# Kernel optimization log

Hardware: AMD Instinct MI355X
Metric: run time of the kernel (lower is better)

Reference implementation:

```python
import jax, jax.numpy as jnp
import numpy as np
import math

B, S, D, H = 2, 2048, 1024, 16
DH = D // H  # dim_per_head = 64


def setup_inputs() -> dict:
    key = jax.random.key(0)
    ks = jax.random.split(key, 12)
    s = 1.0 / math.sqrt(D)
    return {
        "key": jax.random.normal(ks[0], (B, S, D), jnp.float32),
        "value": jax.random.normal(ks[1], (B, S, D), jnp.float32),
        "query": jax.random.normal(ks[2], (B, S, D), jnp.float32),
        "mask": jax.random.randint(ks[3], (B, S, S), 0, 2).astype(bool),
        "Wq": jax.random.normal(ks[4], (D, D), jnp.float32) * s,
        "bq": jnp.zeros((D,), jnp.float32),
        "Wk": jax.random.normal(ks[5], (D, D), jnp.float32) * s,
        "bk": jnp.zeros((D,), jnp.float32),
        "Wv": jax.random.normal(ks[6], (D, D), jnp.float32) * s,
        "bv": jnp.zeros((D,), jnp.float32),
        "Wo": jax.random.normal(ks[7], (D, D), jnp.float32) * s,
        "bo": jnp.zeros((D,), jnp.float32),
    }


def _shape(x):
    # [B, S, D] -> [B, H, S, DH]
    return x.reshape(B, -1, H, DH).transpose(0, 2, 1, 3)


def reference(key, value, query, mask, Wq, bq, Wk, bk, Wv, bv, Wo, bo):
    q = _shape(query @ Wq.T + bq)  # [B,H,Sq,DH]
    k = _shape(key @ Wk.T + bk)    # [B,H,Sk,DH]
    v = _shape(value @ Wv.T + bv)  # [B,H,Sk,DH]
    q = q / jnp.sqrt(jnp.asarray(DH, q.dtype))
    scores = jnp.einsum("bhqd,bhkd->bhqk", q, k)
    scores = jnp.where(mask[:, None, :, :], jnp.asarray(-1e18, scores.dtype), scores)
    attn = jax.nn.softmax(scores, axis=-1)
    # dropout is identity in eval/deterministic reference
    ctx = jnp.einsum("bhqk,bhkd->bhqd", attn, v)
    ctx = ctx.transpose(0, 2, 1, 3).reshape(B, -1, D)  # unshape
    return ctx @ Wo.T + bo
```

## Files before the change

kernel.cpp:

```cpp
#include <hip/hip_runtime.h>
#include <math.h>


constexpr int Bc  = 2;
constexpr int Sc  = 2048;
constexpr int Dc  = 1024;
constexpr int Hc  = 16;
constexpr int DHc = 64;
constexpr int BSc = Bc * Sc;

constexpr float LOG2E = 1.4426950408889634f;

typedef __bf16 bf16x8 __attribute__((ext_vector_type(8)));
typedef __bf16 bf16x4 __attribute__((ext_vector_type(4)));
typedef __bf16 bf16x2 __attribute__((ext_vector_type(2)));
typedef float  f32x4  __attribute__((ext_vector_type(4)));
typedef float  f32x16 __attribute__((ext_vector_type(16)));
typedef unsigned uint32x2 __attribute__((ext_vector_type(2)));
typedef unsigned uint32x4 __attribute__((ext_vector_type(4)));

#define GLDS16(gp, lp) __builtin_amdgcn_global_load_lds( \
    (const __attribute__((address_space(1))) void*)(gp), \
    (__attribute__((address_space(3))) void*)(lp), 16, 0, 0)

__global__ __launch_bounds__(256)
void wsplit(const float* __restrict__ W0, const float* __restrict__ W1,
            const float* __restrict__ W2, const float* __restrict__ W3,
            __bf16* __restrict__ out, __bf16* __restrict__ out2)
{
    const float* src[4] = {W0, W1, W2, W3};
    const int z = blockIdx.y;
    const size_t idx = ((size_t)blockIdx.x * 256 + threadIdx.x) * 4;
    const float4 v = *(const float4*)&src[z][idx];
    if (z == 3) {
        bf16x8 o;
        o[0] = (__bf16)v.x; o[1] = (__bf16)v.x;
        o[2] = (__bf16)v.y; o[3] = (__bf16)v.y;
        o[4] = (__bf16)v.z; o[5] = (__bf16)v.z;
        o[6] = (__bf16)v.w; o[7] = (__bf16)v.w;
        *(bf16x8*)&out2[idx * 2] = o;
    } else {
        bf16x4 o;
        o[0] = (__bf16)v.x; o[1] = (__bf16)v.y; o[2] = (__bf16)v.z; o[3] = (__bf16)v.w;
        *(bf16x4*)&out[(size_t)z * Dc * Dc + idx] = o;
    }
}

__global__ __launch_bounds__(256)
void acast(const float* __restrict__ A0, const float* __restrict__ A1,
           const float* __restrict__ A2, __bf16* __restrict__ out)
{
    const float* src[3] = {A0, A1, A2};
    const int z = blockIdx.y;
    const size_t idx = ((size_t)blockIdx.x * 256 + threadIdx.x) * 8;
    const float4 a = *(const float4*)&src[z][idx];
    const float4 b = *(const float4*)&src[z][idx + 4];
    bf16x8 o;
    o[0] = (__bf16)a.x; o[1] = (__bf16)a.y; o[2] = (__bf16)a.z; o[3] = (__bf16)a.w;
    o[4] = (__bf16)b.x; o[5] = (__bf16)b.y; o[6] = (__bf16)b.z; o[7] = (__bf16)b.w;
    *(bf16x8*)&out[(size_t)z * BSc * Dc + idx] = o;
}

template<int KD>
__device__ __forceinline__ void sweep128bb(const __bf16* __restrict__ A,
                                           const __bf16* __restrict__ Wh,
                                           char* AsB, char* WsB,
                                           int gm0, int gn0, f32x4 acc[4][4])
{
    const int tid  = threadIdx.x;
    const int w    = tid >> 6;
    const int lane = tid & 63;
    const int cc   = lane & 15;
    const int g    = lane >> 4;
    const int wm   = (w & 1) * 64;
    const int wn   = (w >> 1) * 64;

    int wrow[4], wchk[4];
#pragma unroll
    for (int r = 0; r < 4; ++r) {
        const int L = r * 256 + tid;
        wrow[r] = L >> 3;
        wchk[r] = (L & 7) ^ (wrow[r] & 7);
    }

#pragma unroll
    for (int r = 0; r < 4; ++r) {
        GLDS16(Wh + (size_t)(gn0 + wrow[r]) * KD + wchk[r] * 8,
               WsB + (r * 256 + tid) * 16);
        GLDS16(A + (size_t)(gm0 + wrow[r]) * KD + wchk[r] * 8,
               AsB + (r * 256 + tid) * 16);
    }

    for (int it = 0; it < KD / 64; ++it) {
        const char* As = AsB + (it & 1) * 16384;
        const char* Ws = WsB + (it & 1) * 16384;
        __syncthreads();

        if (it + 1 < KD / 64) {
            const int kn = (it + 1) * 64;
            char* Wn = WsB + ((it + 1) & 1) * 16384;
            char* An = AsB + ((it + 1) & 1) * 16384;
#pragma unroll
            for (int r = 0; r < 4; ++r) {
                GLDS16(Wh + (size_t)(gn0 + wrow[r]) * KD + kn + wchk[r] * 8,
                       Wn + (r * 256 + tid) * 16);
                GLDS16(A + (size_t)(gm0 + wrow[r]) * KD + kn + wchk[r] * 8,
                       An + (r * 256 + tid) * 16);
            }
        }

        __builtin_amdgcn_s_setprio(1);
#pragma unroll
        for (int kk = 0; kk < 2; ++kk) {
            const int cb4 = (kk * 4 + g) << 4;
            bf16x8 af[4], bfr[4];
#pragma unroll
            for (int mt = 0; mt < 4; ++mt) {
                const int row = wm + mt * 16 + cc;
                af[mt] = *(const bf16x8*)(As + row * 128 + (cb4 ^ ((row & 7) << 4)));
            }
#pragma unroll
            for (int nt = 0; nt < 4; ++nt) {
                const int row = wn + nt * 16 + cc;
                bfr[nt] = *(const bf16x8*)(Ws + row * 128 + (cb4 ^ ((row & 7) << 4)));
            }
#pragma unroll
            for (int mt = 0; mt < 4; ++mt)
#pragma unroll
                for (int nt = 0; nt < 4; ++nt)
                    acc[mt][nt] = __builtin_amdgcn_mfma_f32_16x16x32_bf16(
                        af[mt], bfr[nt], acc[mt][nt], 0, 0, 0);
        }
        __builtin_amdgcn_s_setprio(0);
    }
}

__global__ __launch_bounds__(256)
void qkv_mfma(const __bf16* __restrict__ Abf, const __bf16* __restrict__ Whi,
              const float* __restrict__ bq, const float* __restrict__ bk,
              const float* __restrict__ bv,
              __bf16* __restrict__ Qo, __bf16* __restrict__ Ko, __bf16* __restrict__ Vt)
{
    __shared__ __align__(16) char smem[65536];

    const int z = blockIdx.z;
    const float* bias = (z == 0) ? bq : (z == 1) ? bk : bv;
    const float scale = (z == 0) ? 0.125f * LOG2E : 1.0f;
    const __bf16* A   = Abf + (size_t)z * BSc * Dc;
    const __bf16* Wh  = Whi + (size_t)z * Dc * Dc;

    const int gm0 = blockIdx.x * 128;
    const int gn0 = blockIdx.y * 128;

    f32x4 acc[4][4];
#pragma unroll
    for (int mt = 0; mt < 4; ++mt)
#pragma unroll
        for (int nt = 0; nt < 4; ++nt) acc[mt][nt] = {0.f, 0.f, 0.f, 0.f};

    sweep128bb<Dc>(A, Wh, smem, smem + 32768, gm0, gn0, acc);

    const int tid = threadIdx.x;
    const int w = tid >> 6, lane = tid & 63;
    const int cc = lane & 15, g = lane >> 4;
    const int wm = (w & 1) * 64, wn = (w >> 1) * 64;

    float bias4[4];
#pragma unroll
    for (int nt = 0; nt < 4; ++nt) bias4[nt] = bias[gn0 + wn + nt * 16 + cc];

    if (z == 2) {
#pragma unroll
        for (int mt = 0; mt < 4; ++mt)
#pragma unroll
            for (int nt = 0; nt < 4; ++nt) {
                const int col = gn0 + wn + nt * 16 + cc;
                const int h = col >> 6, dh = col & 63;
                const int row0 = gm0 + wm + mt * 16 + g * 4;
                const int b = row0 >> 11, s0 = row0 & 2047;
                bf16x4 vv;
#pragma unroll
                for (int reg = 0; reg < 4; ++reg)
                    vv[reg] = (__bf16)(acc[mt][nt][reg] + bias4[nt]);
                *(bf16x4*)&Vt[(((size_t)(b * Hc + h)) * DHc + dh) * Sc + s0] = vv;
            }
    } else {
        __bf16* O = (z == 0) ? Qo : Ko;
#pragma unroll
        for (int mt = 0; mt < 4; ++mt)
#pragma unroll
            for (int nt = 0; nt < 4; ++nt) {
                const int col = gn0 + wn + nt * 16 + cc;
                const int h = col >> 6, dh = col & 63;
#pragma unroll
                for (int reg = 0; reg < 4; ++reg) {
                    const int row = gm0 + wm + mt * 16 + g * 4 + reg;
                    const int b = row >> 11, s = row & 2047;
                    O[(((size_t)(b * Hc + h)) * Sc + s) * DHc + dh] =
                        (__bf16)((acc[mt][nt][reg] + bias4[nt]) * scale);
                }
            }
    }
}

__global__ __launch_bounds__(256)
void out_mfma(const __bf16* __restrict__ ctx2, const __bf16* __restrict__ Wo2,
              const float* __restrict__ bo, float* __restrict__ out)
{
    __shared__ __align__(16) char smem[65536];

    const int gm0 = blockIdx.x * 128;
    const int gn0 = blockIdx.y * 128;

    f32x4 acc[4][4];
#pragma unroll
    for (int mt = 0; mt < 4; ++mt)
#pragma unroll
        for (int nt = 0; nt < 4; ++nt) acc[mt][nt] = {0.f, 0.f, 0.f, 0.f};

    sweep128bb<2 * Dc>(ctx2, Wo2, smem, smem + 32768, gm0, gn0, acc);

    const int tid = threadIdx.x;
    const int w = tid >> 6, lane = tid & 63;
    const int cc = lane & 15, g = lane >> 4;
    const int wm = (w & 1) * 64, wn = (w >> 1) * 64;

    float bias4[4];
#pragma unroll
    for (int nt = 0; nt < 4; ++nt) bias4[nt] = bo[gn0 + wn + nt * 16 + cc];

#pragma unroll
    for (int mt = 0; mt < 4; ++mt)
#pragma unroll
        for (int nt = 0; nt < 4; ++nt) {
            const int col = gn0 + wn + nt * 16 + cc;
#pragma unroll
            for (int reg = 0; reg < 4; ++reg) {
                const int row = gm0 + wm + mt * 16 + g * 4 + reg;
                out[(size_t)row * Dc + col] = acc[mt][nt][reg] + bias4[nt];
            }
        }
}

__global__ __launch_bounds__(256)
void mask_pack(const int* __restrict__ mask, unsigned long long* __restrict__ out)
{
    const int lane = threadIdx.x & 63;
    const size_t waveBase = ((size_t)blockIdx.x * 4 + (threadIdx.x >> 6)) * 256;
    unsigned long long b0 = __ballot(mask[waveBase + lane]        != 0);
    unsigned long long b1 = __ballot(mask[waveBase + 64 + lane]   != 0);
    unsigned long long b2 = __ballot(mask[waveBase + 128 + lane]  != 0);
    unsigned long long b3 = __ballot(mask[waveBase + 192 + lane]  != 0);
    if (lane == 0) {
        unsigned long long* dst = out + (waveBase >> 6);
        dst[0] = b0; dst[1] = b1; dst[2] = b2; dst[3] = b3;
    }
}

__global__ __launch_bounds__(256, 2)
void attn_mfma(const __bf16* __restrict__ Q, const __bf16* __restrict__ K,
               const __bf16* __restrict__ Vt,
               const unsigned long long* __restrict__ mp,
               __bf16* __restrict__ ctx2)
{
    __shared__ __align__(16) char smem[32768];

    const int tid  = threadIdx.x;
    const int w    = tid >> 6;
    const int lane = tid & 63;
    const int c    = lane & 31;
    const int u    = lane >> 5;
    const int bh   = blockIdx.y;
    const int b    = bh >> 4;
    const int h    = bh & 15;
    const int qw   = blockIdx.x * 128 + w * 32;

    const __bf16* Qb  = Q  + (size_t)bh * Sc * DHc;
    const __bf16* Kb  = K  + (size_t)bh * Sc * DHc;
    const __bf16* Vtb = Vt + (size_t)bh * DHc * Sc;

    bf16x8 qa[4];
#pragma unroll
    for (int ch = 0; ch < 4; ++ch)
        qa[ch] = *(const bf16x8*)&Qb[(size_t)(qw + c) * DHc + ch * 16 + u * 8];

    f32x16 o[2];
#pragma unroll
    for (int dt = 0; dt < 2; ++dt)
#pragma unroll
        for (int i = 0; i < 16; ++i) o[dt][i] = 0.f;
    float lp[4] = {0.f, 0.f, 0.f, 0.f};

    const int ci[2] = {tid, 256 + tid};
    int rowi[2], ski[2];
#pragma unroll
    for (int i = 0; i < 2; ++i) {
        rowi[i] = ci[i] >> 3;
        ski[i]  = (ci[i] & 7) ^ (rowi[i] & 7);
    }

#pragma unroll
    for (int i = 0; i < 2; ++i) {
        GLDS16(Kb + (size_t)rowi[i] * DHc + ski[i] * 8,
               smem + ci[i] * 16);
        GLDS16(Vtb + (size_t)rowi[i] * Sc + ski[i] * 8,
               smem + 8192 + ci[i] * 16);
    }

    for (int it = 0; it < 32; ++it) {
        const char* Ks = smem + (it & 1) * 16384;
        const char* Vs = Ks + 8192;

        __syncthreads();

        if (it + 1 < 32) {
            char* Kn = smem + ((it + 1) & 1) * 16384;
            const int kn = (it + 1) * 64;
#pragma unroll
            for (int i = 0; i < 2; ++i) {
                GLDS16(Kb + (size_t)(kn + rowi[i]) * DHc + ski[i] * 8,
                       Kn + ci[i] * 16);
                GLDS16(Vtb + (size_t)rowi[i] * Sc + kn + ski[i] * 8,
                       Kn + 8192 + ci[i] * 16);
            }
        }

        const unsigned long long mw =
            mp[((size_t)(b * Sc + qw + c) << 5) + it];

        f32x16 sc[2];
        __builtin_amdgcn_s_setprio(1);
#pragma unroll
        for (int nt = 0; nt < 2; ++nt) {
            f32x16 z;
#pragma unroll
            for (int i = 0; i < 16; ++i) z[i] = -24.f;
#pragma unroll
            for (int ch = 0; ch < 4; ++ch) {
                const int row = nt * 32 + c;
                const bf16x8 kb = *(const bf16x8*)
                    (Ks + row * 128 + ((ch * 32 + u * 16) ^ ((row & 7) << 4)));
                z = __builtin_amdgcn_mfma_f32_32x32x16_bf16(kb, qa[ch], z, 0, 0, 0);
            }
            sc[nt] = z;
        }
        __builtin_amdgcn_s_setprio(0);

        unsigned pk[2][4][2];
#pragma unroll
        for (int nt = 0; nt < 2; ++nt)
#pragma unroll
            for (int rr = 0; rr < 4; ++rr) {
                const unsigned nib =
                    (unsigned)(mw >> (nt * 32 + rr * 8 + u * 4)) & 0xFu;
                float pv[4];
#pragma unroll
                for (int r = 0; r < 4; ++r) {
                    float p = __builtin_amdgcn_exp2f(sc[nt][rr * 4 + r]);
                    p = (nib & (1u << r)) ? 0.f : p;
                    lp[rr] += p;
                    pv[r] = p;
                }
                bf16x2 t0; t0[0] = (__bf16)pv[0]; t0[1] = (__bf16)pv[1];
                bf16x2 t1; t1[0] = (__bf16)pv[2]; t1[1] = (__bf16)pv[3];
                pk[nt][rr][0] = __builtin_bit_cast(unsigned, t0);
                pk[nt][rr][1] = __builtin_bit_cast(unsigned, t1);
            }

        bf16x8 pa[4];
#pragma unroll
        for (int kc = 0; kc < 4; ++kc) {
            const int nt = kc >> 1;
            const int r0 = (kc & 1) * 2;
            uint32x2 s0 = __builtin_amdgcn_permlane32_swap(
                pk[nt][r0][0], pk[nt][r0 + 1][0], false, false);
            uint32x2 s1 = __builtin_amdgcn_permlane32_swap(
                pk[nt][r0][1], pk[nt][r0 + 1][1], false, false);
            uint32x4 wds;
            wds[0] = s0[0]; wds[1] = s1[0]; wds[2] = s0[1]; wds[3] = s1[1];
            pa[kc] = __builtin_bit_cast(bf16x8, wds);
        }

        __builtin_amdgcn_s_setprio(1);
#pragma unroll
        for (int dt = 0; dt < 2; ++dt)
#pragma unroll
            for (int kc = 0; kc < 4; ++kc) {
                const int row = dt * 32 + c;
                const bf16x8 vb = *(const bf16x8*)
                    (Vs + row * 128 + ((kc * 32 + u * 16) ^ ((row & 7) << 4)));
                o[dt] = __builtin_amdgcn_mfma_f32_32x32x16_bf16(pa[kc], vb, o[dt], 0, 0, 0);
            }
        __builtin_amdgcn_s_setprio(0);
    }

    float lsum = (lp[0] + lp[1]) + (lp[2] + lp[3]);
    lsum += __shfl_xor(lsum, 32);
    const float linv = 1.0f / lsum;

    float inv[16];
#pragma unroll
    for (int i = 0; i < 16; ++i)
        inv[i] = __shfl(linv, (i & 3) + 8 * (i >> 2) + 4 * u);

#pragma unroll
    for (int dt = 0; dt < 2; ++dt)
#pragma unroll
        for (int i = 0; i < 16; ++i) {
            const int q = qw + (i & 3) + 8 * (i >> 2) + 4 * u;
            const int col = h * 64 + dt * 32 + c;
            const float v = o[dt][i] * inv[i];
            const __bf16 hi = (__bf16)v;
            bf16x2 hv;
            hv[0] = hi;
            hv[1] = (__bf16)(v - (float)hi);
            *(bf16x2*)&ctx2[(((size_t)b * Sc + q) * Dc + col) * 2] = hv;
        }
}

extern "C" void kernel_launch(void* const* d_in, const int* in_sizes, int n_in,
                              void* d_out, int out_size, void* d_ws, size_t ws_size,
                              hipStream_t stream)
{
    const float* key   = (const float*)d_in[0];
    const float* value = (const float*)d_in[1];
    const float* query = (const float*)d_in[2];
    const int*   mask  = (const int*)  d_in[3];
    const float* Wq    = (const float*)d_in[4];
    const float* bq    = (const float*)d_in[5];
    const float* Wk    = (const float*)d_in[6];
    const float* bk    = (const float*)d_in[7];
    const float* Wv    = (const float*)d_in[8];
    const float* bv    = (const float*)d_in[9];
    const float* Wo    = (const float*)d_in[10];
    const float* bo    = (const float*)d_in[11];
    float* out = (float*)d_out;

    char* wsb = (char*)d_ws;
    __bf16* Qbf  = (__bf16*)(wsb);
    __bf16* Kbf  = (__bf16*)(wsb + ((size_t)8  << 20));
    __bf16* Vt   = (__bf16*)(wsb + ((size_t)16 << 20));
    unsigned long long* mpk = (unsigned long long*)(wsb + ((size_t)24 << 20));
    __bf16* Whi  = (__bf16*)(wsb + ((size_t)25 << 20));
    __bf16* Wo2  = (__bf16*)(wsb + ((size_t)31 << 20));
    __bf16* ctx2 = (__bf16*)(wsb + ((size_t)35 << 20));
    __bf16* Abf  = (__bf16*)(wsb + ((size_t)51 << 20));

    dim3 gws(Dc * Dc / (256 * 4), 4);
    wsplit<<<gws, 256, 0, stream>>>(Wq, Wk, Wv, Wo, Whi, Wo2);

    dim3 gac(BSc * Dc / (256 * 8), 3);
    acast<<<gac, 256, 0, stream>>>(query, key, value, Abf);

    dim3 gqkv(BSc / 128, Dc / 128, 3);
    qkv_mfma<<<gqkv, 256, 0, stream>>>(Abf, Whi, bq, bk, bv, Qbf, Kbf, Vt);

    const int mask_n = Bc * Sc * Sc;
    mask_pack<<<mask_n / 1024, 256, 0, stream>>>(mask, mpk);

    dim3 gattn(Sc / 128, Bc * Hc);
    attn_mfma<<<gattn, 256, 0, stream>>>(Qbf, Kbf, Vt, mpk, ctx2);

    dim3 gout(BSc / 128, Dc / 128);
    out_mfma<<<gout, 256, 0, stream>>>(ctx2, Wo2, bo, out);
}
```

Baseline: 268.1 us.

## Use 64-row tiles for output GEMM and split MFMA accumulator chains in attention

The output projection moves from 128x128 to 64x128 tiles through a new sweep64bb helper, which doubles the block count (256 to 512) for better CU occupancy on the K=2048 GEMM. In the attention kernel, the QK^T and PV MFMA chains are split across two independent accumulators that are summed afterwards, so dependent MFMAs can overlap. The cost is more reloading of the weight tile across blocks and extra accumulator registers, which may reduce attention occupancy.

```diff
diff --git a/kernel.cpp b/kernel.cpp
--- a/kernel.cpp
+++ b/kernel.cpp
@@ -135,6 +135,89 @@
     }
 }
 
+template<int KD>
+__device__ __forceinline__ void sweep64bb(const __bf16* __restrict__ A,
+                                          const __bf16* __restrict__ Wh,
+                                          char* AsB, char* WsB,
+                                          int gm0, int gn0, f32x4 acc[2][4])
+{
+    const int tid  = threadIdx.x;
+    const int w    = tid >> 6;
+    const int lane = tid & 63;
+    const int cc   = lane & 15;
+    const int g    = lane >> 4;
+    const int wm   = (w & 1) * 32;
+    const int wn   = (w >> 1) * 64;
+
+    int wrow[4], wchk[4];
+#pragma unroll
+    for (int r = 0; r < 4; ++r) {
+        const int L = r * 256 + tid;
+        wrow[r] = L >> 3;
+        wchk[r] = (L & 7) ^ (wrow[r] & 7);
+    }
+    int arow[2], achk[2];
+#pragma unroll
+    for (int r = 0; r < 2; ++r) {
+        const int L = r * 256 + tid;
+        arow[r] = L >> 3;
+        achk[r] = (L & 7) ^ (arow[r] & 7);
+    }
+
+#pragma unroll
+    for (int r = 0; r < 4; ++r)
+        GLDS16(Wh + (size_t)(gn0 + wrow[r]) * KD + wchk[r] * 8,
+               WsB + (r * 256 + tid) * 16);
+#pragma unroll
+    for (int r = 0; r < 2; ++r)
+        GLDS16(A + (size_t)(gm0 + arow[r]) * KD + achk[r] * 8,
+               AsB + (r * 256 + tid) * 16);
+
+    for (int it = 0; it < KD / 64; ++it) {
+        const char* As = AsB + (it & 1) * 8192;
+        const char* Ws = WsB + (it & 1) * 16384;
+        __syncthreads();
+
+        if (it + 1 < KD / 64) {
+            const int kn = (it + 1) * 64;
+            char* Wn = WsB + ((it + 1) & 1) * 16384;
+            char* An = AsB + ((it + 1) & 1) * 8192;
+#pragma unroll
+            for (int r = 0; r < 4; ++r)
+                GLDS16(Wh + (size_t)(gn0 + wrow[r]) * KD + kn + wchk[r] * 8,
+                       Wn + (r * 256 + tid) * 16);
+#pragma unroll
+            for (int r = 0; r < 2; ++r)
+                GLDS16(A + (size_t)(gm0 + arow[r]) * KD + kn + achk[r] * 8,
+                       An + (r * 256 + tid) * 16);
+        }
+
+        __builtin_amdgcn_s_setprio(1);
+#pragma unroll
+        for (int kk = 0; kk < 2; ++kk) {
+            const int cb4 = (kk * 4 + g) << 4;
+            bf16x8 af[2], bfr[4];
+#pragma unroll
+            for (int mt = 0; mt < 2; ++mt) {
+                const int row = wm + mt * 16 + cc;
+                af[mt] = *(const bf16x8*)(As + row * 128 + (cb4 ^ ((row & 7) << 4)));
+            }
+#pragma unroll
+            for (int nt = 0; nt < 4; ++nt) {
+                const int row = wn + nt * 16 + cc;
+                bfr[nt] = *(const bf16x8*)(Ws + row * 128 + (cb4 ^ ((row & 7) << 4)));
+            }
+#pragma unroll
+            for (int mt = 0; mt < 2; ++mt)
+#pragma unroll
+                for (int nt = 0; nt < 4; ++nt)
+                    acc[mt][nt] = __builtin_amdgcn_mfma_f32_16x16x32_bf16(
+                        af[mt], bfr[nt], acc[mt][nt], 0, 0, 0);
+        }
+        __builtin_amdgcn_s_setprio(0);
+    }
+}
+
 __global__ __launch_bounds__(256)
 void qkv_mfma(const __bf16* __restrict__ Abf, const __bf16* __restrict__ Whi,
               const float* __restrict__ bq, const float* __restrict__ bk,
@@ -207,30 +290,30 @@
 void out_mfma(const __bf16* __restrict__ ctx2, const __bf16* __restrict__ Wo2,
               const float* __restrict__ bo, float* __restrict__ out)
 {
-    __shared__ __align__(16) char smem[65536];
-
-    const int gm0 = blockIdx.x * 128;
+    __shared__ __align__(16) char smem[49152];
+
+    const int gm0 = blockIdx.x * 64;
     const int gn0 = blockIdx.y * 128;
 
-    f32x4 acc[4][4];
-#pragma unroll
-    for (int mt = 0; mt < 4; ++mt)
+    f32x4 acc[2][4];
+#pragma unroll
+    for (int mt = 0; mt < 2; ++mt)
 #pragma unroll
         for (int nt = 0; nt < 4; ++nt) acc[mt][nt] = {0.f, 0.f, 0.f, 0.f};
 
-    sweep128bb<2 * Dc>(ctx2, Wo2, smem, smem + 32768, gm0, gn0, acc);
+    sweep64bb<2 * Dc>(ctx2, Wo2, smem + 32768, smem, gm0, gn0, acc);
 
     const int tid = threadIdx.x;
     const int w = tid >> 6, lane = tid & 63;
     const int cc = lane & 15, g = lane >> 4;
-    const int wm = (w & 1) * 64, wn = (w >> 1) * 64;
+    const int wm = (w & 1) * 32, wn = (w >> 1) * 64;
 
     float bias4[4];
 #pragma unroll
     for (int nt = 0; nt < 4; ++nt) bias4[nt] = bo[gn0 + wn + nt * 16 + cc];
 
 #pragma unroll
-    for (int mt = 0; mt < 4; ++mt)
+    for (int mt = 0; mt < 2; ++mt)
 #pragma unroll
         for (int nt = 0; nt < 4; ++nt) {
             const int col = gn0 + wn + nt * 16 + cc;
@@ -284,11 +367,11 @@
     for (int ch = 0; ch < 4; ++ch)
         qa[ch] = *(const bf16x8*)&Qb[(size_t)(qw + c) * DHc + ch * 16 + u * 8];
 
-    f32x16 o[2];
+    f32x16 o[2], o2[2];
 #pragma unroll
     for (int dt = 0; dt < 2; ++dt)
 #pragma unroll
-        for (int i = 0; i < 16; ++i) o[dt][i] = 0.f;
+        for (int i = 0; i < 16; ++i) { o[dt][i] = 0.f; o2[dt][i] = 0.f; }
     float lp[4] = {0.f, 0.f, 0.f, 0.f};
 
     const int ci[2] = {tid, 256 + tid};
@@ -332,17 +415,20 @@
         __builtin_amdgcn_s_setprio(1);
 #pragma unroll
         for (int nt = 0; nt < 2; ++nt) {
-            f32x16 z;
-#pragma unroll
-            for (int i = 0; i < 16; ++i) z[i] = -24.f;
-#pragma unroll
-            for (int ch = 0; ch < 4; ++ch) {
-                const int row = nt * 32 + c;
-                const bf16x8 kb = *(const bf16x8*)
-                    (Ks + row * 128 + ((ch * 32 + u * 16) ^ ((row & 7) << 4)));
-                z = __builtin_amdgcn_mfma_f32_32x32x16_bf16(kb, qa[ch], z, 0, 0, 0);
-            }
-            sc[nt] = z;
+            f32x16 z0, z1;
+#pragma unroll
+            for (int i = 0; i < 16; ++i) { z0[i] = -24.f; z1[i] = 0.f; }
+            const int row = nt * 32 + c;
+            const int rx  = (row & 7) << 4;
+            const bf16x8 kb0 = *(const bf16x8*)(Ks + row * 128 + ((0  + u * 16) ^ rx));
+            const bf16x8 kb1 = *(const bf16x8*)(Ks + row * 128 + ((32 + u * 16) ^ rx));
+            const bf16x8 kb2 = *(const bf16x8*)(Ks + row * 128 + ((64 + u * 16) ^ rx));
+            const bf16x8 kb3 = *(const bf16x8*)(Ks + row * 128 + ((96 + u * 16) ^ rx));
+            z0 = __builtin_amdgcn_mfma_f32_32x32x16_bf16(kb0, qa[0], z0, 0, 0, 0);
+            z1 = __builtin_amdgcn_mfma_f32_32x32x16_bf16(kb1, qa[1], z1, 0, 0, 0);
+            z0 = __builtin_amdgcn_mfma_f32_32x32x16_bf16(kb2, qa[2], z0, 0, 0, 0);
+            z1 = __builtin_amdgcn_mfma_f32_32x32x16_bf16(kb3, qa[3], z1, 0, 0, 0);
+            sc[nt] = z0 + z1;
         }
         __builtin_amdgcn_s_setprio(0);
 
@@ -383,14 +469,18 @@
 
         __builtin_amdgcn_s_setprio(1);
 #pragma unroll
-        for (int dt = 0; dt < 2; ++dt)
-#pragma unroll
-            for (int kc = 0; kc < 4; ++kc) {
-                const int row = dt * 32 + c;
-                const bf16x8 vb = *(const bf16x8*)
-                    (Vs + row * 128 + ((kc * 32 + u * 16) ^ ((row & 7) << 4)));
-                o[dt] = __builtin_amdgcn_mfma_f32_32x32x16_bf16(pa[kc], vb, o[dt], 0, 0, 0);
-            }
+        for (int dt = 0; dt < 2; ++dt) {
+            const int row = dt * 32 + c;
+            const int rx  = (row & 7) << 4;
+            const bf16x8 vb0 = *(const bf16x8*)(Vs + row * 128 + ((0  + u * 16) ^ rx));
+            const bf16x8 vb1 = *(const bf16x8*)(Vs + row * 128 + ((32 + u * 16) ^ rx));
+            const bf16x8 vb2 = *(const bf16x8*)(Vs + row * 128 + ((64 + u * 16) ^ rx));
+            const bf16x8 vb3 = *(const bf16x8*)(Vs + row * 128 + ((96 + u * 16) ^ rx));
+            o[dt]  = __builtin_amdgcn_mfma_f32_32x32x16_bf16(pa[0], vb0, o[dt],  0, 0, 0);
+            o2[dt] = __builtin_amdgcn_mfma_f32_32x32x16_bf16(pa[1], vb1, o2[dt], 0, 0, 0);
+            o[dt]  = __builtin_amdgcn_mfma_f32_32x32x16_bf16(pa[2], vb2, o[dt],  0, 0, 0);
+            o2[dt] = __builtin_amdgcn_mfma_f32_32x32x16_bf16(pa[3], vb3, o2[dt], 0, 0, 0);
+        }
         __builtin_amdgcn_s_setprio(0);
     }
 
@@ -409,7 +499,7 @@
         for (int i = 0; i < 16; ++i) {
             const int q = qw + (i & 3) + 8 * (i >> 2) + 4 * u;
             const int col = h * 64 + dt * 32 + c;
-            const float v = o[dt][i] * inv[i];
+            const float v = (o[dt][i] + o2[dt][i]) * inv[i];
             const __bf16 hi = (__bf16)v;
             bf16x2 hv;
             hv[0] = hi;
@@ -461,6 +551,6 @@
     dim3 gattn(Sc / 128, Bc * Hc);
     attn_mfma<<<gattn, 256, 0, stream>>>(Qbf, Kbf, Vt, mpk, ctx2);
 
-    dim3 gout(BSc / 128, Dc / 128);
+    dim3 gout(BSc / 64, Dc / 128);
     out_mfma<<<gout, 256, 0, stream>>>(ctx2, Wo2, bo, out);
 }
```

New measurement: 267.4 us. Within noise of the previous version (-0.2%).
